# Kernel optimization log

Hardware: AMD Instinct MI355X
Metric: run time of the kernel (lower is better)

The kernel has to match this reference:

```python
import math
import jax, jax.numpy as jnp
import numpy as np

LM_DAMPING = 1e-3
MOTION_LAMBDA = 1.0
LM_ITERS = (2, 3, 4)


def _skew(w):  # (B,3) -> (B,3,3)
    z = jnp.zeros_like(w[:, 0])
    return jnp.stack([z, -w[:, 2], w[:, 1],
                      w[:, 2], z, -w[:, 0],
                      -w[:, 1], w[:, 0], z], axis=-1).reshape(-1, 3, 3)


def _se3_exp(xi):  # (B,6) -> (B,4,4)
    t, w = xi[:, :3], xi[:, 3:]
    theta = jnp.clip(jnp.linalg.norm(w, axis=-1, keepdims=True), 1e-8, None)  # (B,1)
    K = _skew(w / theta)
    eye = jnp.eye(3, dtype=xi.dtype)
    st = jnp.sin(theta)[:, :, None]          # (B,1,1)
    ct = (1.0 - jnp.cos(theta))[:, :, None]
    KK = K @ K
    R = eye + st * K + ct * KK
    th = jnp.clip(theta[:, :, None], 1e-8, None)
    V = eye + (ct / th) * K + (1.0 - st / th) * KK
    t_out = (V @ t[..., None])[..., 0]
    B = xi.shape[0]
    T = jnp.tile(jnp.eye(4, dtype=xi.dtype)[None], (B, 1, 1))
    T = T.at[:, :3, :3].set(R).at[:, :3, 3].set(t_out)
    return T


def _se3_log(T):  # (B,4,4) -> (B,6)
    R, t = T[:, :3, :3], T[:, :3, 3]
    cos_a = (R[:, 0, 0] + R[:, 1, 1] + R[:, 2, 2] - 1.0) / 2.0
    theta = jnp.arccos(jnp.clip(cos_a, -1.0 + 1e-7, 1.0 - 1e-7))
    small = jnp.abs(theta) < 1e-6
    th = jnp.clip(theta, 1e-8, None)
    w = jnp.stack([R[:, 2, 1] - R[:, 1, 2],
                   R[:, 0, 2] - R[:, 2, 0],
                   R[:, 1, 0] - R[:, 0, 1]], axis=-1)
    w = w / (2.0 * jnp.clip(jnp.sin(th), 1e-8, None))[:, None] * th[:, None]
    w = jnp.where(small[:, None], 0.0, w)
    return jnp.concatenate([t, w], axis=-1)


def _sample_one(feat, gx, gy):
    # feat (C,H,W); gx,gy (P,) normalized in [-1,1]; align_corners=False, border padding
    C, H, W = feat.shape
    x = jnp.clip(((gx + 1.0) * W - 1.0) / 2.0, 0.0, W - 1)
    y = jnp.clip(((gy + 1.0) * H - 1.0) / 2.0, 0.0, H - 1)
    x0 = jnp.floor(x); y0 = jnp.floor(y)
    x1 = jnp.minimum(x0 + 1.0, W - 1); y1 = jnp.minimum(y0 + 1.0, H - 1)
    wx = x - x0; wy = y - y0
    x0i, x1i = x0.astype(jnp.int32), x1.astype(jnp.int32)
    y0i, y1i = y0.astype(jnp.int32), y1.astype(jnp.int32)
    f00 = feat[:, y0i, x0i]; f01 = feat[:, y0i, x1i]
    f10 = feat[:, y1i, x0i]; f11 = feat[:, y1i, x1i]
    return (f00 * (1 - wx) * (1 - wy) + f01 * wx * (1 - wy)
            + f10 * (1 - wx) * wy + f11 * wx * wy)  # (C,P)

_sample = jax.vmap(_sample_one, in_axes=(0, 0, 0))


def _generate_hypotheses(T_pred, key):
    rng = jnp.arange(-11.0, 13.0, 2.0, dtype=jnp.float32)  # 12 values
    pg, yg = jnp.meshgrid(rng, rng, indexing='ij')
    pitch = pg.reshape(-1) * (math.pi / 180.0)
    yaw = yg.reshape(-1) * (math.pi / 180.0)
    M = pitch.shape[0]  # 144
    t_noise = jax.random.normal(key, (M, 3), dtype=jnp.float32) * 1.0  # translation_std
    xi = jnp.stack([t_noise[:, 0], t_noise[:, 1], t_noise[:, 2],
                    jnp.zeros(M, jnp.float32), pitch, yaw], axis=-1)
    dT = _se3_exp(xi)  # (M,4,4)
    return jnp.einsum('mij,bjk->bmik', dT, T_pred)  # (B,M,4,4)


def _residuals(T, q_feat, r_feat, q_unc, geo, K, level):
    # T (B,M,4,4); fallback path evaluates only first min(M,16) hypotheses
    B, M = T.shape[:2]
    _, C, H, W = q_feat.shape
    scale = 1.0 / (4.0 / 2 ** level)
    Ks = jnp.concatenate([K[:, :2] * scale, K[:, 2:]], axis=1)
    M16 = min(M, 16)
    Tm = T[:, :M16]  # (B,16,4,4)
    N = geo.shape[1]
    pts_h = jnp.concatenate([geo, jnp.ones((B, N, 1), geo.dtype)], axis=-1)  # (B,N,4)
    pts_cam = jnp.einsum('bmij,bnj->bmni', Tm[:, :, :3, :], pts_h)  # (B,16,N,3)
    z = jnp.clip(pts_cam[..., 2:3], 1e-6, None)
    xy = pts_cam[..., :2] / z
    fx = Ks[:, 0, 0][:, None, None]; fy = Ks[:, 1, 1][:, None, None]
    cx = Ks[:, 0, 2][:, None, None]; cy = Ks[:, 1, 2][:, None, None]
    u = fx * xy[..., 0] + cx
    v = fy * xy[..., 1] + cy
    gx = (2.0 * u / max(W - 1, 1) - 1.0).reshape(B, M16 * N)
    gy = (2.0 * v / max(H - 1, 1) - 1.0).reshape(B, M16 * N)
    qs = _sample(q_feat, gx, gy).reshape(B, C, M16, N)
    rs = _sample(r_feat, gx, gy).reshape(B, C, M16, N)
    diff2 = (qs - rs) ** 2
    unc = _sample(q_unc, gx, gy).reshape(B, 1, M16, N)
    res = (diff2 * unc).sum(axis=1).mean(axis=-1)  # (B,16)
    return jnp.zeros((B, M), T.dtype).at[:, :M16].set(res)


def reference(T_pred, geo_anchors, intrinsics, q0, q1, q2, r0, r1, r2, u0, u1, u2):
    key = jax.random.key(42)
    B = T_pred.shape[0]
    T_cur = _generate_hypotheses(T_pred, jax.random.fold_in(key, 0))
    M = T_cur.shape[1]
    q_feats = (q0, q1, q2); r_feats = (r0, r1, r2); uncs = (u0, u1, u2)
    costs = jnp.zeros((B, M), T_pred.dtype)
    for level, n_iters in enumerate(LM_ITERS):
        for it in range(n_iters):
            res = _residuals(T_cur, q_feats[level], r_feats[level], uncs[level],
                             geo_anchors, intrinsics, level)
            damping = LM_DAMPING * 0.5 ** level
            noise = jax.random.normal(jax.random.fold_in(key, 100 + level * 10 + it),
                                      (B, M, 6), dtype=T_pred.dtype)
            step = -damping * res[..., None] * noise * 0.01
            delta = _se3_exp(step.reshape(B * M, 6)).reshape(B, M, 4, 4)
            T_cur = delta @ T_cur
            costs = res
    # motion-constrained selection: C_total = C_photo + lambda * ||log(T_ref T_pred^-1)||
    T_rel = T_cur @ jnp.linalg.inv(T_pred)[:, None]
    geod = jnp.linalg.norm(_se3_log(T_rel.reshape(B * M, 4, 4)), axis=-1).reshape(B, M)
    total = costs + MOTION_LAMBDA * geod
    idx = jnp.argmin(total, axis=1)
    T_best = jnp.take_along_axis(T_cur, idx[:, None, None, None], axis=1)[:, 0]
    return T_best, costs


def setup_inputs() -> dict:
    key = jax.random.key(0)
    ks = jax.random.split(key, 16)
    B, N = 8, 500
    # valid SE(3) predicted poses (small perturbation of identity)
    T_pred = _se3_exp(jax.random.normal(ks[0], (B, 6), jnp.float32) * 0.1)
    # 3D anchors in front of the camera (z ~ 6)
    geo = jax.random.uniform(ks[1], (B, N, 3), jnp.float32, -2.0, 2.0)
    geo = geo.at[..., 2].add(6.0)
    K = jnp.tile(jnp.array([[200.0, 0.0, 128.0],
                            [0.0, 200.0, 96.0],
                            [0.0, 0.0, 1.0]], jnp.float32)[None], (B, 1, 1))
    shapes_f = [(B, 128, 48, 64), (B, 64, 96, 128), (B, 32, 192, 256)]
    q = [jax.random.normal(ks[2 + i], s, jnp.float32) for i, s in enumerate(shapes_f)]
    r = [jax.random.normal(ks[5 + i], s, jnp.float32) for i, s in enumerate(shapes_f)]
    u = [jax.random.uniform(ks[8 + i], (s[0], 1, s[2], s[3]), jnp.float32)
         for i, s in enumerate(shapes_f)]
    return {"T_pred": T_pred, "geo_anchors": geo, "intrinsics": K,
            "q0": q[0], "q1": q[1], "q2": q[2],
            "r0": r[0], "r1": r[1], "r2": r[2],
            "u0": u[0], "u1": u[1], "u2": u[2]}
```

## Files before the change

### kernel.cpp

```cpp
#include <hip/hip_runtime.h>
#include <stdint.h>
#include <math.h>

#define JAX_PARTITIONABLE 1

#define NB 8
#define NM 144
#define NM16 16
#define NPTS 500
#define GP 16

__host__ __device__ __forceinline__ uint32_t rotl32(uint32_t x, int r) {
    return (x << r) | (x >> (32 - r));
}

__host__ __device__ inline void threefry2x32(uint32_t k0, uint32_t k1,
                                             uint32_t x0, uint32_t x1,
                                             uint32_t& o0, uint32_t& o1) {
    uint32_t ks2 = k0 ^ k1 ^ 0x1BD11BDAu;
    x0 += k0; x1 += k1;
    const int RA[4] = {13, 15, 26, 6};
    const int RB[4] = {17, 29, 16, 24};
#define R4(ROT) { x0 += x1; x1 = rotl32(x1, ROT[0]); x1 ^= x0; \
                  x0 += x1; x1 = rotl32(x1, ROT[1]); x1 ^= x0; \
                  x0 += x1; x1 = rotl32(x1, ROT[2]); x1 ^= x0; \
                  x0 += x1; x1 = rotl32(x1, ROT[3]); x1 ^= x0; }
    R4(RA); x0 += k1;  x1 += ks2 + 1u;
    R4(RB); x0 += ks2; x1 += k0 + 2u;
    R4(RA); x0 += k0;  x1 += k1 + 3u;
    R4(RB); x0 += k1;  x1 += ks2 + 4u;
    R4(RA); x0 += ks2; x1 += k0 + 5u;
#undef R4
    o0 = x0; o1 = x1;
}

__device__ __forceinline__ float erfinv32(float x) {
    float w = -log1pf(-x * x);
    float p;
    if (w < 5.0f) {
        w = w - 2.5f;
        p = 2.81022636e-08f;
        p = fmaf(p, w, 3.43273939e-07f);
        p = fmaf(p, w, -3.5233877e-06f);
        p = fmaf(p, w, -4.39150654e-06f);
        p = fmaf(p, w, 0.00021858087f);
        p = fmaf(p, w, -0.00125372503f);
        p = fmaf(p, w, -0.00417768164f);
        p = fmaf(p, w, 0.246640727f);
        p = fmaf(p, w, 1.50140941f);
    } else {
        w = sqrtf(w) - 3.0f;
        p = -0.000200214257f;
        p = fmaf(p, w, 0.000100950558f);
        p = fmaf(p, w, 0.00134934322f);
        p = fmaf(p, w, -0.00367342844f);
        p = fmaf(p, w, 0.00573950773f);
        p = fmaf(p, w, -0.0076224613f);
        p = fmaf(p, w, 0.00943887047f);
        p = fmaf(p, w, 1.00167406f);
        p = fmaf(p, w, 2.83297682f);
    }
    return p * x;
}

__device__ __forceinline__ float jax_normal(uint32_t k0, uint32_t k1,
                                            uint32_t idx, uint32_t half) {
    uint32_t o0, o1, bits;
#if JAX_PARTITIONABLE
    threefry2x32(k0, k1, 0u, idx, o0, o1);
    bits = o0 ^ o1;
#else
    if (idx < half) { threefry2x32(k0, k1, idx, idx + half, o0, o1); bits = o0; }
    else            { threefry2x32(k0, k1, idx - half, idx, o0, o1); bits = o1; }
#endif
    uint32_t fb = (bits >> 9) | 0x3F800000u;
    float f = __uint_as_float(fb) - 1.0f;
    const float lo = -0.99999994f;
    float u = f * (1.0f - lo) + lo;
    u = fmaxf(lo, u);
    return 1.4142135623730951f * erfinv32(u);
}

__device__ inline void se3_exp6(const float xi[6], float T[12]) {
    float tx = xi[0], ty = xi[1], tz = xi[2];
    float wx = xi[3], wy = xi[4], wz = xi[5];
    float nrm = sqrtf(wx * wx + wy * wy + wz * wz);
    float theta = fmaxf(nrm, 1e-8f);
    float kx = wx / theta, ky = wy / theta, kz = wz / theta;
    float K[9] = {0.0f, -kz, ky, kz, 0.0f, -kx, -ky, kx, 0.0f};
    float st = sinf(theta);
    float ct = 1.0f - cosf(theta);
    float KK[9];
    for (int i = 0; i < 3; i++)
        for (int j = 0; j < 3; j++)
            KK[i * 3 + j] = K[i * 3 + 0] * K[0 + j] + K[i * 3 + 1] * K[3 + j] + K[i * 3 + 2] * K[6 + j];
    float a = ct / theta;
    float bb = 1.0f - st / theta;
    float R[9], V[9];
    for (int i = 0; i < 3; i++)
        for (int j = 0; j < 3; j++) {
            float e = (i == j) ? 1.0f : 0.0f;
            R[i * 3 + j] = e + st * K[i * 3 + j] + ct * KK[i * 3 + j];
            V[i * 3 + j] = e + a * K[i * 3 + j] + bb * KK[i * 3 + j];
        }
    float t0 = V[0] * tx + V[1] * ty + V[2] * tz;
    float t1 = V[3] * tx + V[4] * ty + V[5] * tz;
    float t2 = V[6] * tx + V[7] * ty + V[8] * tz;
    T[0] = R[0]; T[1] = R[1]; T[2] = R[2];  T[3] = t0;
    T[4] = R[3]; T[5] = R[4]; T[6] = R[5];  T[7] = t1;
    T[8] = R[6]; T[9] = R[7]; T[10] = R[8]; T[11] = t2;
}

__device__ inline void compose44(const float dT[12], const float P[16], float Tn[16]) {
    for (int i = 0; i < 3; i++)
        for (int j = 0; j < 4; j++)
            Tn[i * 4 + j] = dT[i * 4 + 0] * P[0 + j] + dT[i * 4 + 1] * P[4 + j] +
                            dT[i * 4 + 2] * P[8 + j] + dT[i * 4 + 3] * P[12 + j];
    Tn[12] = 0.0f; Tn[13] = 0.0f; Tn[14] = 0.0f; Tn[15] = 1.0f;
}

__device__ inline void make_hypothesis(int m, const float* P, uint32_t hk0, uint32_t hk1,
                                       float Tn[16]) {
    float tn[3];
    for (int c = 0; c < 3; c++)
        tn[c] = jax_normal(hk0, hk1, (uint32_t)(m * 3 + c), 216u);
    int gi = m / 12, gj = m % 12;
    const float d2r = (float)(M_PI / 180.0);
    float xi[6] = {tn[0], tn[1], tn[2], 0.0f,
                   (float)(2 * gi - 11) * d2r, (float)(2 * gj - 11) * d2r};
    float dT[12];
    se3_exp6(xi, dT);
    compose44(dT, P, Tn);
}

__device__ inline void se3_exp6d(const double xi[6], double T[12]) {
    double tx = xi[0], ty = xi[1], tz = xi[2];
    double wx = xi[3], wy = xi[4], wz = xi[5];
    double nrm = sqrt(wx * wx + wy * wy + wz * wz);
    double theta = fmax(nrm, 1e-8);
    double kx = wx / theta, ky = wy / theta, kz = wz / theta;
    double K[9] = {0.0, -kz, ky, kz, 0.0, -kx, -ky, kx, 0.0};
    double st = sin(theta);
    double ct = 1.0 - cos(theta);
    double KK[9];
    for (int i = 0; i < 3; i++)
        for (int j = 0; j < 3; j++)
            KK[i * 3 + j] = K[i * 3 + 0] * K[0 + j] + K[i * 3 + 1] * K[3 + j] + K[i * 3 + 2] * K[6 + j];
    double a = ct / theta;
    double bb = 1.0 - st / theta;
    double R[9], V[9];
    for (int i = 0; i < 3; i++)
        for (int j = 0; j < 3; j++) {
            double e = (i == j) ? 1.0 : 0.0;
            R[i * 3 + j] = e + st * K[i * 3 + j] + ct * KK[i * 3 + j];
            V[i * 3 + j] = e + a * K[i * 3 + j] + bb * KK[i * 3 + j];
        }
    double t0 = V[0] * tx + V[1] * ty + V[2] * tz;
    double t1 = V[3] * tx + V[4] * ty + V[5] * tz;
    double t2 = V[6] * tx + V[7] * ty + V[8] * tz;
    T[0] = R[0]; T[1] = R[1]; T[2] = R[2];  T[3] = t0;
    T[4] = R[3]; T[5] = R[4]; T[6] = R[5];  T[7] = t1;
    T[8] = R[6]; T[9] = R[7]; T[10] = R[8]; T[11] = t2;
}

__device__ inline void compose44d(const double dT[12], const double P[16], double Tn[16]) {
    for (int i = 0; i < 3; i++)
        for (int j = 0; j < 4; j++)
            Tn[i * 4 + j] = dT[i * 4 + 0] * P[0 + j] + dT[i * 4 + 1] * P[4 + j] +
                            dT[i * 4 + 2] * P[8 + j] + dT[i * 4 + 3] * P[12 + j];
    Tn[12] = 0.0; Tn[13] = 0.0; Tn[14] = 0.0; Tn[15] = 1.0;
}

__device__ inline void make_hypothesis_d(int m, const double* P, uint32_t hk0, uint32_t hk1,
                                         double Tn[16]) {
    float tn[3];
    for (int c = 0; c < 3; c++)
        tn[c] = jax_normal(hk0, hk1, (uint32_t)(m * 3 + c), 216u);
    int gi = m / 12, gj = m % 12;
    const float d2r = (float)(M_PI / 180.0);
    float pf = (float)(2 * gi - 11) * d2r;
    float yf = (float)(2 * gj - 11) * d2r;
    double xi[6] = {(double)tn[0], (double)tn[1], (double)tn[2], 0.0,
                    (double)pf, (double)yf};
    double dT[12];
    se3_exp6d(xi, dT);
    compose44d(dT, P, Tn);
}

struct IterKeys { uint32_t k0[9]; uint32_t k1[9]; float damping[9]; };

template <int C, int H, int W, int GRP>
__device__ void gram_body_v(const float* __restrict__ q, const float* __restrict__ r,
                            const float* __restrict__ u, float* __restrict__ G,
                            float* part, int blk) {
    constexpr int HW = H * W;
    constexpr int PT = 256 / GRP;
    constexpr int PPB = PT * 4;
    constexpr int TPB = HW / PPB;
    constexpr int CPG = C / GRP;
    const int b = blk / TPB;
    const int tile = blk % TPB;
    const int tid = threadIdx.x;
    const int g = tid / PT;
    const int p = tid % PT;
    const int px0 = tile * PPB + p * 4;
    const int y = px0 / W;
    const int x0 = px0 - y * W;
    const int y1 = (y + 1 < H) ? y + 1 : H - 1;
    const bool edge = (x0 + 4 >= W);

    const int rb0 = y * W + x0;
    const int rb1 = y1 * W + x0;
    const float* qp = q + ((size_t)b * C + (size_t)g * CPG) * HW;
    const float* rp = r + ((size_t)b * C + (size_t)g * CPG) * HW;

    float acc[4][10];
#pragma unroll
    for (int j = 0; j < 4; j++)
#pragma unroll
        for (int i = 0; i < 10; i++) acc[j][i] = 0.0f;

#pragma unroll 2
    for (int c = 0; c < CPG; c++) {
        float4 a0 = *(const float4*)(qp + rb0);
        float4 a1 = *(const float4*)(qp + rb1);
        float4 b0 = *(const float4*)(rp + rb0);
        float4 b1 = *(const float4*)(rp + rb1);
        qp += HW; rp += HW;
        float e0[5], e1[5];
        e0[0] = a0.x - b0.x; e0[1] = a0.y - b0.y; e0[2] = a0.z - b0.z; e0[3] = a0.w - b0.w;
        e1[0] = a1.x - b1.x; e1[1] = a1.y - b1.y; e1[2] = a1.z - b1.z; e1[3] = a1.w - b1.w;
        float d0n = __shfl_down(e0[0], 1, 64);
        float d1n = __shfl_down(e1[0], 1, 64);
        e0[4] = edge ? e0[3] : d0n;
        e1[4] = edge ? e1[3] : d1n;
#pragma unroll
        for (int j = 0; j < 4; j++) {
            float d00 = e0[j], d01 = e0[j + 1];
            float d10 = e1[j], d11 = e1[j + 1];
            acc[j][0] = fmaf(d00, d00, acc[j][0]);
            acc[j][1] = fmaf(d00, d01, acc[j][1]);
            acc[j][2] = fmaf(d00, d10, acc[j][2]);
            acc[j][3] = fmaf(d00, d11, acc[j][3]);
            acc[j][4] = fmaf(d01, d01, acc[j][4]);
            acc[j][5] = fmaf(d01, d10, acc[j][5]);
            acc[j][6] = fmaf(d01, d11, acc[j][6]);
            acc[j][7] = fmaf(d10, d10, acc[j][7]);
            acc[j][8] = fmaf(d10, d11, acc[j][8]);
            acc[j][9] = fmaf(d11, d11, acc[j][9]);
        }
    }
    if (GRP > 1) {
        if (g > 0) {
            float* pp = part + (size_t)(g - 1) * 40 * PT;
#pragma unroll
            for (int j = 0; j < 4; j++)
#pragma unroll
                for (int i = 0; i < 10; i++)
                    pp[(j * 10 + i) * PT + p] = acc[j][i];
        }
        __syncthreads();
        if (g == 0) {
            for (int gg = 1; gg < GRP; gg++) {
                const float* pp = part + (size_t)(gg - 1) * 40 * PT;
#pragma unroll
                for (int j = 0; j < 4; j++)
#pragma unroll
                    for (int i = 0; i < 10; i++)
                        acc[j][i] += pp[(j * 10 + i) * PT + p];
            }
        }
    }
    if (g == 0) {
        const float* ub = u + (size_t)b * HW;
        float4 u0 = *(const float4*)(ub + rb0);
        float4 u1 = *(const float4*)(ub + rb1);
        float w0[5], w1[5];
        w0[0] = u0.x; w0[1] = u0.y; w0[2] = u0.z; w0[3] = u0.w;
        w1[0] = u1.x; w1[1] = u1.y; w1[2] = u1.z; w1[3] = u1.w;
        float u0n = __shfl_down(u0.x, 1, 64);
        float u1n = __shfl_down(u1.x, 1, 64);
        w0[4] = edge ? w0[3] : u0n;
        w1[4] = edge ? w1[3] : u1n;
#pragma unroll
        for (int j = 0; j < 4; j++) {
            size_t base = ((size_t)b * HW + px0 + j) * GP;
            float4 g0v = {acc[j][0], acc[j][1], acc[j][2], acc[j][3]};
            float4 g1v = {acc[j][4], acc[j][5], acc[j][6], acc[j][7]};
            float4 g2v = {acc[j][8], acc[j][9], w0[j], w0[j + 1]};
            float4 g3v = {w1[j], w1[j + 1], 0.0f, 0.0f};
            *(float4*)(G + base + 0)  = g0v;
            *(float4*)(G + base + 4)  = g1v;
            *(float4*)(G + base + 8)  = g2v;
            *(float4*)(G + base + 12) = g3v;
        }
    }
}

#define VBLK0 96
#define VBLK1 192
#define VBLK2 384

__global__ __launch_bounds__(256) void gram_fused_kernel(
    const float* __restrict__ q0, const float* __restrict__ r0, const float* __restrict__ u0,
    float* __restrict__ G0,
    const float* __restrict__ q1, const float* __restrict__ r1, const float* __restrict__ u1,
    float* __restrict__ G1,
    const float* __restrict__ q2, const float* __restrict__ r2, const float* __restrict__ u2,
    float* __restrict__ G2) {
    __shared__ float part[3 * 40 * 64];
    const int blk = blockIdx.x;
    if (blk < VBLK0)
        gram_body_v<128, 48, 64, 4>(q0, r0, u0, G0, part, blk);
    else if (blk < VBLK0 + VBLK1)
        gram_body_v<64, 96, 128, 2>(q1, r1, u1, G1, part, blk - VBLK0);
    else
        gram_body_v<32, 192, 256, 1>(q2, r2, u2, G2, part, blk - VBLK0 - VBLK1);
}

template <int H, int W>
__device__ void run_level_gram(const float* __restrict__ Gb,
                               float fx, float fy, float cx, float cy,
                               const float* geoS, float* Tsh, float* red, float* resS,
                               float* stepS, float* out, int b, int m,
                               const IterKeys& iks, int firstIter, int niter) {
    const int tid = threadIdx.x;
    for (int it = 0; it < niter; it++) {
        const int iter = firstIter + it;
        float acc = 0.0f;
        if (tid < NPTS) {
            float px = geoS[tid * 3], py = geoS[tid * 3 + 1], pz = geoS[tid * 3 + 2];
            float X = Tsh[0] * px + Tsh[1] * py + Tsh[2]  * pz + Tsh[3];
            float Y = Tsh[4] * px + Tsh[5] * py + Tsh[6]  * pz + Tsh[7];
            float Z = Tsh[8] * px + Tsh[9] * py + Tsh[10] * pz + Tsh[11];
            float z = fmaxf(Z, 1e-6f);
            float uu = fx * (X / z) + cx;
            float vv = fy * (Y / z) + cy;
            float gx = 2.0f * uu / (float)(W - 1) - 1.0f;
            float gy = 2.0f * vv / (float)(H - 1) - 1.0f;
            float x = fminf(fmaxf(((gx + 1.0f) * (float)W - 1.0f) * 0.5f, 0.0f), (float)(W - 1));
            float y = fminf(fmaxf(((gy + 1.0f) * (float)H - 1.0f) * 0.5f, 0.0f), (float)(H - 1));
            float x0f = floorf(x), y0f = floorf(y);
            float wx = x - x0f, wy = y - y0f;
            int x0i = (int)x0f, y0i = (int)y0f;
            int i00 = y0i * W + x0i;
            float w00 = (1.0f - wx) * (1.0f - wy), w01 = wx * (1.0f - wy);
            float w10 = (1.0f - wx) * wy,          w11 = wx * wy;
            const float* Gp = Gb + (size_t)i00 * GP;
            float4 g0 = *(const float4*)(Gp + 0);
            float4 g1 = *(const float4*)(Gp + 4);
            float4 g2 = *(const float4*)(Gp + 8);
            float4 g3 = *(const float4*)(Gp + 12);
            float uval = w00 * g2.z + w01 * g2.w + w10 * g3.x + w11 * g3.y;
            float val = w00 * w00 * g0.x + w01 * w01 * g1.x +
                        w10 * w10 * g1.w + w11 * w11 * g2.y +
                        2.0f * (w00 * w01 * g0.y + w00 * w10 * g0.z + w00 * w11 * g0.w +
                                w01 * w10 * g1.y + w01 * w11 * g1.z + w10 * w11 * g2.x);
            acc = uval * val;
        }
        float v = acc;
        for (int off = 32; off > 0; off >>= 1) v += __shfl_down(v, off, 64);
        if ((tid & 63) == 0) red[tid >> 6] = v;
        __syncthreads();
        if (tid == 0) {
            float s = 0.0f;
            for (int w = 0; w < 8; w++) s += red[w];
            float res = s / 500.0f;
            *resS = res;
            if (iter == 8) out[128 + b * NM + m] = res;
        }
        __syncthreads();
        if (tid < 6) {
            uint32_t fi = (uint32_t)((b * NM + m) * 6 + tid);
            float nz = jax_normal(iks.k0[iter], iks.k1[iter], fi, 3456u);
            stepS[tid] = (((-iks.damping[iter]) * (*resS)) * nz) * 0.01f;
        }
        __syncthreads();
        if (tid == 0) {
            float xi[6];
            for (int j = 0; j < 6; j++) xi[j] = stepS[j];
            float dT[12];
            se3_exp6(xi, dT);
            float Told[16];
            for (int k = 0; k < 16; k++) Told[k] = Tsh[k];
            float Tn[16];
            compose44(dT, Told, Tn);
            for (int k = 0; k < 16; k++) Tsh[k] = Tn[k];
        }
        __syncthreads();
    }
}

__global__ __launch_bounds__(512) void evolve_kernel_gram(
    const float* __restrict__ T_pred, const float* __restrict__ geo,
    const float* __restrict__ Kmat,
    const float* __restrict__ G0, const float* __restrict__ G1, const float* __restrict__ G2,
    float* __restrict__ Tws, float* __restrict__ out,
    uint32_t hk0, uint32_t hk1, IterKeys iks) {
    const int bm = blockIdx.x;
    const int b = bm & 7;
    const int m = bm >> 3;
    const int tid = threadIdx.x;

    __shared__ float Tsh[16];
    __shared__ float geoS[NPTS * 3];
    __shared__ float red[8];
    __shared__ float resS;
    __shared__ float stepS[6];

    for (int i = tid; i < NPTS * 3; i += 512) geoS[i] = geo[b * NPTS * 3 + i];

    if (tid == 0) {
        float P[16];
        for (int k = 0; k < 16; k++) P[k] = T_pred[b * 16 + k];
        float Tn[16];
        make_hypothesis(m, P, hk0, hk1, Tn);
        for (int k = 0; k < 16; k++) Tsh[k] = Tn[k];
    }
    __syncthreads();

    float K00 = Kmat[b * 9 + 0], K02 = Kmat[b * 9 + 2];
    float K11 = Kmat[b * 9 + 4], K12 = Kmat[b * 9 + 5];

    run_level_gram<48, 64>(G0 + (size_t)b * 48 * 64 * GP,
                           K00 * 0.25f, K11 * 0.25f, K02 * 0.25f, K12 * 0.25f,
                           geoS, Tsh, red, &resS, stepS, out, b, m, iks, 0, 2);
    run_level_gram<96, 128>(G1 + (size_t)b * 96 * 128 * GP,
                            K00 * 0.5f, K11 * 0.5f, K02 * 0.5f, K12 * 0.5f,
                            geoS, Tsh, red, &resS, stepS, out, b, m, iks, 2, 3);
    run_level_gram<192, 256>(G2 + (size_t)b * 192 * 256 * GP,
                             K00, K11, K02, K12,
                             geoS, Tsh, red, &resS, stepS, out, b, m, iks, 5, 4);

    if (tid < 16) Tws[(size_t)(b * NM16 + m) * 16 + tid] = Tsh[tid];
}

template <int C, int H, int W>
__device__ void run_level_nchw(const float* __restrict__ qb, const float* __restrict__ rb,
                               const float* __restrict__ ub,
                               float fx, float fy, float cx, float cy,
                               const float* geoS, float* Tsh, float* red, float* resS,
                               float* stepS, float* out, int b, int m,
                               const IterKeys& iks, int firstIter, int niter) {
    const int tid = threadIdx.x;
    const int HW = H * W;
    for (int it = 0; it < niter; it++) {
        const int iter = firstIter + it;
        float acc = 0.0f;
        if (tid < NPTS) {
            float px = geoS[tid * 3], py = geoS[tid * 3 + 1], pz = geoS[tid * 3 + 2];
            float X = Tsh[0] * px + Tsh[1] * py + Tsh[2]  * pz + Tsh[3];
            float Y = Tsh[4] * px + Tsh[5] * py + Tsh[6]  * pz + Tsh[7];
            float Z = Tsh[8] * px + Tsh[9] * py + Tsh[10] * pz + Tsh[11];
            float z = fmaxf(Z, 1e-6f);
            float uu = fx * (X / z) + cx;
            float vv = fy * (Y / z) + cy;
            float gx = 2.0f * uu / (float)(W - 1) - 1.0f;
            float gy = 2.0f * vv / (float)(H - 1) - 1.0f;
            float x = fminf(fmaxf(((gx + 1.0f) * (float)W - 1.0f) * 0.5f, 0.0f), (float)(W - 1));
            float y = fminf(fmaxf(((gy + 1.0f) * (float)H - 1.0f) * 0.5f, 0.0f), (float)(H - 1));
            float x0f = floorf(x), y0f = floorf(y);
            float x1f = fminf(x0f + 1.0f, (float)(W - 1));
            float y1f = fminf(y0f + 1.0f, (float)(H - 1));
            float wx = x - x0f, wy = y - y0f;
            int x0i = (int)x0f, x1i = (int)x1f, y0i = (int)y0f, y1i = (int)y1f;
            int i00 = y0i * W + x0i, i01 = y0i * W + x1i;
            int i10 = y1i * W + x0i, i11 = y1i * W + x1i;
            float w00 = (1.0f - wx) * (1.0f - wy), w01 = wx * (1.0f - wy);
            float w10 = (1.0f - wx) * wy,          w11 = wx * wy;
            float uval = ub[i00] * w00 + ub[i01] * w01 + ub[i10] * w10 + ub[i11] * w11;
            const float* qp = qb;
            const float* rp = rb;
#pragma unroll 4
            for (int c = 0; c < C; c++) {
                float qv = qp[i00] * w00 + qp[i01] * w01 + qp[i10] * w10 + qp[i11] * w11;
                float rv = rp[i00] * w00 + rp[i01] * w01 + rp[i10] * w10 + rp[i11] * w11;
                float d = qv - rv;
                acc += uval * (d * d);
                qp += HW; rp += HW;
            }
        }
        float v = acc;
        for (int off = 32; off > 0; off >>= 1) v += __shfl_down(v, off, 64);
        if ((tid & 63) == 0) red[tid >> 6] = v;
        __syncthreads();
        if (tid == 0) {
            float s = 0.0f;
            for (int w = 0; w < 8; w++) s += red[w];
            float res = s / 500.0f;
            *resS = res;
            if (iter == 8) out[128 + b * NM + m] = res;
        }
        __syncthreads();
        if (tid < 6) {
            uint32_t fi = (uint32_t)((b * NM + m) * 6 + tid);
            float nz = jax_normal(iks.k0[iter], iks.k1[iter], fi, 3456u);
            stepS[tid] = (((-iks.damping[iter]) * (*resS)) * nz) * 0.01f;
        }
        __syncthreads();
        if (tid == 0) {
            float xi[6];
            for (int j = 0; j < 6; j++) xi[j] = stepS[j];
            float dT[12];
            se3_exp6(xi, dT);
            float Told[16];
            for (int k = 0; k < 16; k++) Told[k] = Tsh[k];
            float Tn[16];
            compose44(dT, Told, Tn);
            for (int k = 0; k < 16; k++) Tsh[k] = Tn[k];
        }
        __syncthreads();
    }
}

__global__ __launch_bounds__(512) void evolve_kernel_nchw(
    const float* __restrict__ T_pred, const float* __restrict__ geo,
    const float* __restrict__ Kmat,
    const float* __restrict__ q0, const float* __restrict__ q1, const float* __restrict__ q2,
    const float* __restrict__ r0, const float* __restrict__ r1, const float* __restrict__ r2,
    const float* __restrict__ u0, const float* __restrict__ u1, const float* __restrict__ u2,
    float* __restrict__ Tws, float* __restrict__ out,
    uint32_t hk0, uint32_t hk1, IterKeys iks) {
    const int bm = blockIdx.x;
    const int b = bm >> 4;
    const int m = bm & 15;
    const int tid = threadIdx.x;

    __shared__ float Tsh[16];
    __shared__ float geoS[NPTS * 3];
    __shared__ float red[8];
    __shared__ float resS;
    __shared__ float stepS[6];

    for (int i = tid; i < NPTS * 3; i += 512) geoS[i] = geo[b * NPTS * 3 + i];

    if (tid == 0) {
        float P[16];
        for (int k = 0; k < 16; k++) P[k] = T_pred[b * 16 + k];
        float Tn[16];
        make_hypothesis(m, P, hk0, hk1, Tn);
        for (int k = 0; k < 16; k++) Tsh[k] = Tn[k];
    }
    __syncthreads();

    float K00 = Kmat[b * 9 + 0], K02 = Kmat[b * 9 + 2];
    float K11 = Kmat[b * 9 + 4], K12 = Kmat[b * 9 + 5];

    run_level_nchw<128, 48, 64>(q0 + (size_t)b * 128 * 48 * 64, r0 + (size_t)b * 128 * 48 * 64,
                                u0 + (size_t)b * 48 * 64,
                                K00 * 0.25f, K11 * 0.25f, K02 * 0.25f, K12 * 0.25f,
                                geoS, Tsh, red, &resS, stepS, out, b, m, iks, 0, 2);
    run_level_nchw<64, 96, 128>(q1 + (size_t)b * 64 * 96 * 128, r1 + (size_t)b * 64 * 96 * 128,
                                u1 + (size_t)b * 96 * 128,
                                K00 * 0.5f, K11 * 0.5f, K02 * 0.5f, K12 * 0.5f,
                                geoS, Tsh, red, &resS, stepS, out, b, m, iks, 2, 3);
    run_level_nchw<32, 192, 256>(q2 + (size_t)b * 32 * 192 * 256, r2 + (size_t)b * 32 * 192 * 256,
                                 u2 + (size_t)b * 192 * 256,
                                 K00, K11, K02, K12,
                                 geoS, Tsh, red, &resS, stepS, out, b, m, iks, 5, 4);

    if (tid < 16) Tws[(size_t)bm * 16 + tid] = Tsh[tid];
}

__global__ __launch_bounds__(192) void finalize_kernel(
    const float* __restrict__ T_pred, const float* __restrict__ Tws,
    float* __restrict__ out, uint32_t hk0, uint32_t hk1) {
    const int b = blockIdx.x;
    const int tid = threadIdx.x;
    __shared__ double Pm[16];
    __shared__ double inv[12];
    __shared__ double totals[NM];
    __shared__ int bestm_sh;

    if (tid < 16) Pm[tid] = (double)T_pred[b * 16 + tid];
    __syncthreads();
    if (tid == 0) {
        for (int k = 0; k < 3; k++)
            for (int j = 0; j < 3; j++) inv[k * 4 + j] = Pm[j * 4 + k];
        for (int k = 0; k < 3; k++)
            inv[k * 4 + 3] = -(Pm[0 * 4 + k] * Pm[3] + Pm[1 * 4 + k] * Pm[7] + Pm[2 * 4 + k] * Pm[11]);
    }
    __syncthreads();

    double Tc[16];
    if (tid < NM) {
        double cost;
        if (tid < NM16) {
            for (int k = 0; k < 16; k++) Tc[k] = (double)Tws[(size_t)(b * NM16 + tid) * 16 + k];
            cost = (double)out[128 + b * NM + tid];
        } else {
            make_hypothesis_d(tid, Pm, hk0, hk1, Tc);
            cost = 0.0;
            out[128 + b * NM + tid] = 0.0f;
        }
        double Tr[12];
        for (int i = 0; i < 3; i++)
            for (int j = 0; j < 4; j++)
                Tr[i * 4 + j] = Tc[i * 4 + 0] * inv[0 + j] + Tc[i * 4 + 1] * inv[4 + j] +
                                Tc[i * 4 + 2] * inv[8 + j] + ((j == 3) ? Tc[i * 4 + 3] : 0.0);
        double cos_a = (Tr[0] + Tr[5] + Tr[10] - 1.0) * 0.5;
        cos_a = fmin(fmax(cos_a, -1.0 + 1e-7), 1.0 - 1e-7);
        double theta = acos(cos_a);
        double th = fmax(theta, 1e-8);
        double s2 = 2.0 * fmax(sin(th), 1e-8);
        double w0 = (Tr[2 * 4 + 1] - Tr[1 * 4 + 2]) / s2 * th;
        double w1 = (Tr[0 * 4 + 2] - Tr[2 * 4 + 0]) / s2 * th;
        double w2 = (Tr[1 * 4 + 0] - Tr[0 * 4 + 1]) / s2 * th;
        double t0 = Tr[3], t1 = Tr[7], t2 = Tr[11];
        double geod = sqrt(t0 * t0 + t1 * t1 + t2 * t2 + w0 * w0 + w1 * w1 + w2 * w2);
        totals[tid] = cost + geod;
    }
    __syncthreads();
    if (tid == 0) {
        int best = 0;
        double bv = totals[0];
        for (int mm = 1; mm < NM; mm++) {
            if (totals[mm] < bv) { bv = totals[mm]; best = mm; }
        }
        bestm_sh = best;
    }
    __syncthreads();
    if (tid == bestm_sh) {
        for (int k = 0; k < 16; k++) out[b * 16 + k] = (float)Tc[k];
    }
}

extern "C" void kernel_launch(void* const* d_in, const int* in_sizes, int n_in,
                              void* d_out, int out_size, void* d_ws, size_t ws_size,
                              hipStream_t stream) {
    (void)in_sizes; (void)n_in; (void)out_size;
    const float* T_pred = (const float*)d_in[0];
    const float* geo    = (const float*)d_in[1];
    const float* K      = (const float*)d_in[2];
    const float* q0 = (const float*)d_in[3];
    const float* q1 = (const float*)d_in[4];
    const float* q2 = (const float*)d_in[5];
    const float* r0 = (const float*)d_in[6];
    const float* r1 = (const float*)d_in[7];
    const float* r2 = (const float*)d_in[8];
    const float* u0 = (const float*)d_in[9];
    const float* u1 = (const float*)d_in[10];
    const float* u2 = (const float*)d_in[11];
    float* out = (float*)d_out;

    float* Tws = (float*)d_ws;
    const size_t nG0 = (size_t)NB * 48 * 64 * GP;
    const size_t nG1 = (size_t)NB * 96 * 128 * GP;
    const size_t nG2 = (size_t)NB * 192 * 256 * GP;
    float* G0 = Tws + 2048;
    float* G1 = G0 + nG0;
    float* G2 = G1 + nG1;
    const size_t need = (2048 + nG0 + nG1 + nG2) * sizeof(float);

    uint32_t hk0, hk1;
    threefry2x32(0u, 42u, 0u, 0u, hk0, hk1);
    IterKeys iks;
    const int seeds[9] = {100, 101, 110, 111, 112, 120, 121, 122, 123};
    const float damp[9] = {0.001f, 0.001f, 0.0005f, 0.0005f, 0.0005f,
                           0.00025f, 0.00025f, 0.00025f, 0.00025f};
    for (int i = 0; i < 9; i++) {
        threefry2x32(0u, 42u, 0u, (uint32_t)seeds[i], iks.k0[i], iks.k1[i]);
        iks.damping[i] = damp[i];
    }

    if (ws_size >= need) {
        gram_fused_kernel<<<dim3(VBLK0 + VBLK1 + VBLK2), dim3(256), 0, stream>>>(
            q0, r0, u0, G0, q1, r1, u1, G1, q2, r2, u2, G2);
        evolve_kernel_gram<<<dim3(NB * NM16), dim3(512), 0, stream>>>(
            T_pred, geo, K, G0, G1, G2, Tws, out, hk0, hk1, iks);
    } else {
        evolve_kernel_nchw<<<dim3(NB * NM16), dim3(512), 0, stream>>>(
            T_pred, geo, K, q0, q1, q2, r0, r1, r2, u0, u1, u2, Tws, out, hk0, hk1, iks);
    }
    finalize_kernel<<<dim3(NB), dim3(192), 0, stream>>>(T_pred, Tws, out, hk0, hk1);
}
```

Measured before the change: 256.9 us.

## Prefetch gram inputs with nontemporal loads and precompute noise per block

The gram kernel's channel loop is now software-pipelined with two register buffers, and uses nontemporal vector loads so the streamed q/r features do not pollute the cache. In the evolve kernel, all 54 Gaussian noise values and the damping factors are computed once up front into shared memory, removing the per-iteration RNG call. The per-iteration step is now computed by the first wavefront through shuffles, dropping two block-wide barriers per iteration. The costs are higher register pressure in the gram loop and extra startup work in each evolve block.

```diff
diff --git a/kernel.cpp b/kernel.cpp
--- a/kernel.cpp
+++ b/kernel.cpp
@@ -9,6 +9,12 @@
 #define NM16 16
 #define NPTS 500
 #define GP 16
+
+typedef float v4f __attribute__((ext_vector_type(4)));
+
+__device__ __forceinline__ v4f nt4(const float* p) {
+    return __builtin_nontemporal_load((const v4f*)p);
+}
 
 __host__ __device__ __forceinline__ uint32_t rotl32(uint32_t x, int r) {
     return (x << r) | (x >> (32 - r));
@@ -220,36 +226,52 @@
 #pragma unroll
         for (int i = 0; i < 10; i++) acc[j][i] = 0.0f;
 
-#pragma unroll 2
-    for (int c = 0; c < CPG; c++) {
-        float4 a0 = *(const float4*)(qp + rb0);
-        float4 a1 = *(const float4*)(qp + rb1);
-        float4 b0 = *(const float4*)(rp + rb0);
-        float4 b1 = *(const float4*)(rp + rb1);
+#define GBODY(A0, A1, B0, B1)                                                  \
+    {                                                                          \
+        float e0[5], e1[5];                                                    \
+        e0[0] = A0.x - B0.x; e0[1] = A0.y - B0.y;                              \
+        e0[2] = A0.z - B0.z; e0[3] = A0.w - B0.w;                              \
+        e1[0] = A1.x - B1.x; e1[1] = A1.y - B1.y;                              \
+        e1[2] = A1.z - B1.z; e1[3] = A1.w - B1.w;                              \
+        float d0n = __shfl_down(e0[0], 1, 64);                                 \
+        float d1n = __shfl_down(e1[0], 1, 64);                                 \
+        e0[4] = edge ? e0[3] : d0n;                                            \
+        e1[4] = edge ? e1[3] : d1n;                                            \
+        _Pragma("unroll")                                                      \
+        for (int j = 0; j < 4; j++) {                                          \
+            float d00 = e0[j], d01 = e0[j + 1];                                \
+            float d10 = e1[j], d11 = e1[j + 1];                                \
+            acc[j][0] = fmaf(d00, d00, acc[j][0]);                             \
+            acc[j][1] = fmaf(d00, d01, acc[j][1]);                             \
+            acc[j][2] = fmaf(d00, d10, acc[j][2]);                             \
+            acc[j][3] = fmaf(d00, d11, acc[j][3]);                             \
+            acc[j][4] = fmaf(d01, d01, acc[j][4]);                             \
+            acc[j][5] = fmaf(d01, d10, acc[j][5]);                             \
+            acc[j][6] = fmaf(d01, d11, acc[j][6]);                             \
+            acc[j][7] = fmaf(d10, d10, acc[j][7]);                             \
+            acc[j][8] = fmaf(d10, d11, acc[j][8]);                             \
+            acc[j][9] = fmaf(d11, d11, acc[j][9]);                             \
+        }                                                                      \
+    }
+
+    v4f a0A, a1A, b0A, b1A, a0B, a1B, b0B, b1B;
+    a0A = nt4(qp + rb0); a1A = nt4(qp + rb1);
+    b0A = nt4(rp + rb0); b1A = nt4(rp + rb1);
+    qp += HW; rp += HW;
+    for (int c = 0; c < CPG; c += 2) {
+        a0B = nt4(qp + rb0); a1B = nt4(qp + rb1);
+        b0B = nt4(rp + rb0); b1B = nt4(rp + rb1);
         qp += HW; rp += HW;
-        float e0[5], e1[5];
-        e0[0] = a0.x - b0.x; e0[1] = a0.y - b0.y; e0[2] = a0.z - b0.z; e0[3] = a0.w - b0.w;
-        e1[0] = a1.x - b1.x; e1[1] = a1.y - b1.y; e1[2] = a1.z - b1.z; e1[3] = a1.w - b1.w;
-        float d0n = __shfl_down(e0[0], 1, 64);
-        float d1n = __shfl_down(e1[0], 1, 64);
-        e0[4] = edge ? e0[3] : d0n;
-        e1[4] = edge ? e1[3] : d1n;
-#pragma unroll
-        for (int j = 0; j < 4; j++) {
-            float d00 = e0[j], d01 = e0[j + 1];
-            float d10 = e1[j], d11 = e1[j + 1];
-            acc[j][0] = fmaf(d00, d00, acc[j][0]);
-            acc[j][1] = fmaf(d00, d01, acc[j][1]);
-            acc[j][2] = fmaf(d00, d10, acc[j][2]);
-            acc[j][3] = fmaf(d00, d11, acc[j][3]);
-            acc[j][4] = fmaf(d01, d01, acc[j][4]);
-            acc[j][5] = fmaf(d01, d10, acc[j][5]);
-            acc[j][6] = fmaf(d01, d11, acc[j][6]);
-            acc[j][7] = fmaf(d10, d10, acc[j][7]);
-            acc[j][8] = fmaf(d10, d11, acc[j][8]);
-            acc[j][9] = fmaf(d11, d11, acc[j][9]);
-        }
-    }
+        GBODY(a0A, a1A, b0A, b1A);
+        if (c + 2 < CPG) {
+            a0A = nt4(qp + rb0); a1A = nt4(qp + rb1);
+            b0A = nt4(rp + rb0); b1A = nt4(rp + rb1);
+            qp += HW; rp += HW;
+        }
+        GBODY(a0B, a1B, b0B, b1B);
+    }
+#undef GBODY
+
     if (GRP > 1) {
         if (g > 0) {
             float* pp = part + (size_t)(g - 1) * 40 * PT;
@@ -321,9 +343,9 @@
 template <int H, int W>
 __device__ void run_level_gram(const float* __restrict__ Gb,
                                float fx, float fy, float cx, float cy,
-                               const float* geoS, float* Tsh, float* red, float* resS,
-                               float* stepS, float* out, int b, int m,
-                               const IterKeys& iks, int firstIter, int niter) {
+                               const float* geoS, float* Tsh, float* red,
+                               const float* nzS, const float* damping,
+                               float* out, int b, int m, int firstIter, int niter) {
     const int tid = threadIdx.x;
     for (int it = 0; it < niter; it++) {
         const int iter = firstIter + it;
@@ -362,30 +384,26 @@
         for (int off = 32; off > 0; off >>= 1) v += __shfl_down(v, off, 64);
         if ((tid & 63) == 0) red[tid >> 6] = v;
         __syncthreads();
-        if (tid == 0) {
+        if (tid < 64) {
             float s = 0.0f;
             for (int w = 0; w < 8; w++) s += red[w];
             float res = s / 500.0f;
-            *resS = res;
-            if (iter == 8) out[128 + b * NM + m] = res;
-        }
-        __syncthreads();
-        if (tid < 6) {
-            uint32_t fi = (uint32_t)((b * NM + m) * 6 + tid);
-            float nz = jax_normal(iks.k0[iter], iks.k1[iter], fi, 3456u);
-            stepS[tid] = (((-iks.damping[iter]) * (*resS)) * nz) * 0.01f;
-        }
-        __syncthreads();
-        if (tid == 0) {
+            if (tid == 0 && iter == 8) out[128 + b * NM + m] = res;
+            float st = 0.0f;
+            if (tid < 6)
+                st = (((-damping[iter]) * res) * nzS[iter * 6 + tid]) * 0.01f;
             float xi[6];
-            for (int j = 0; j < 6; j++) xi[j] = stepS[j];
-            float dT[12];
-            se3_exp6(xi, dT);
-            float Told[16];
-            for (int k = 0; k < 16; k++) Told[k] = Tsh[k];
-            float Tn[16];
-            compose44(dT, Told, Tn);
-            for (int k = 0; k < 16; k++) Tsh[k] = Tn[k];
+#pragma unroll
+            for (int j = 0; j < 6; j++) xi[j] = __shfl(st, j, 64);
+            if (tid == 0) {
+                float dT[12];
+                se3_exp6(xi, dT);
+                float Told[16];
+                for (int k = 0; k < 16; k++) Told[k] = Tsh[k];
+                float Tn[16];
+                compose44(dT, Told, Tn);
+                for (int k = 0; k < 16; k++) Tsh[k] = Tn[k];
+            }
         }
         __syncthreads();
     }
@@ -405,12 +423,19 @@
     __shared__ float Tsh[16];
     __shared__ float geoS[NPTS * 3];
     __shared__ float red[8];
-    __shared__ float resS;
-    __shared__ float stepS[6];
+    __shared__ float nzS[54];
+    __shared__ float dampS[9];
 
     for (int i = tid; i < NPTS * 3; i += 512) geoS[i] = geo[b * NPTS * 3 + i];
 
-    if (tid == 0) {
+    if (tid < 54) {
+        int it9 = tid / 6, jj = tid % 6;
+        uint32_t fi = (uint32_t)((b * NM + m) * 6 + jj);
+        nzS[tid] = jax_normal(iks.k0[it9], iks.k1[it9], fi, 3456u);
+    }
+    if (tid >= 54 && tid < 63) dampS[tid - 54] = iks.damping[tid - 54];
+
+    if (tid == 64) {
         float P[16];
         for (int k = 0; k < 16; k++) P[k] = T_pred[b * 16 + k];
         float Tn[16];
@@ -424,13 +449,13 @@
 
     run_level_gram<48, 64>(G0 + (size_t)b * 48 * 64 * GP,
                            K00 * 0.25f, K11 * 0.25f, K02 * 0.25f, K12 * 0.25f,
-                           geoS, Tsh, red, &resS, stepS, out, b, m, iks, 0, 2);
+                           geoS, Tsh, red, nzS, dampS, out, b, m, 0, 2);
     run_level_gram<96, 128>(G1 + (size_t)b * 96 * 128 * GP,
                             K00 * 0.5f, K11 * 0.5f, K02 * 0.5f, K12 * 0.5f,
-                            geoS, Tsh, red, &resS, stepS, out, b, m, iks, 2, 3);
+                            geoS, Tsh, red, nzS, dampS, out, b, m, 2, 3);
     run_level_gram<192, 256>(G2 + (size_t)b * 192 * 256 * GP,
                              K00, K11, K02, K12,
-                             geoS, Tsh, red, &resS, stepS, out, b, m, iks, 5, 4);
+                             geoS, Tsh, red, nzS, dampS, out, b, m, 5, 4);
 
     if (tid < 16) Tws[(size_t)(b * NM16 + m) * 16 + tid] = Tsh[tid];
 }
```

Result: faster. 242.9 us (-5.5%).
